# Optimization experiments

Hardware: AMD Instinct MI355X
Metric: run time of the kernel (lower is better)

Reference implementation:

```python
import jax, jax.numpy as jnp
import numpy as np


def _nn_idx(query, ref):
    """Index of nearest ref point for each query point.
    query: [B,N,3], ref: [B,M,3] -> idx [B,N] (int32).
    Squared distance via ||q||^2 - 2 q.r + ||r||^2 (matches cdist+top1).
    """
    d2 = (jnp.sum(query * query, axis=-1, keepdims=True)
          - 2.0 * jnp.einsum('bnd,bmd->bnm', query, ref)
          + jnp.sum(ref * ref, axis=-1)[:, None, :])
    return jnp.argmin(d2, axis=-1)


def setup_inputs() -> dict:
    key = jax.random.key(0)
    k1, k2, k3 = jax.random.split(key, 3)
    B, N, M = 1, 16384, 16384  # batch hard-coded to 1 in original loops
    pred = jax.random.normal(k1, (B, N, 3), dtype=jnp.float32)
    gt = jax.random.normal(k2, (B, M, 3), dtype=jnp.float32)
    weight = jax.random.uniform(k3, (1,), dtype=jnp.float32)
    return {"pred": pred, "gt": gt, "weight": weight}


def reference(pred, gt, weight):
    # get_mse_loss2: weighted bidirectional nearest-neighbor MSE.
    w = weight[0]
    # B2A: align each pred point to its nearest gt point
    idx = _nn_idx(pred, gt)                                   # [B,N]
    align_gt = jnp.take_along_axis(gt, idx[..., None], axis=1)  # [B,N,3]
    B2A = jnp.mean((pred - align_gt) ** 2)
    # A2B: align each gt point to its nearest pred point
    idx2 = _nn_idx(gt, pred)                                  # [B,M]
    align_out = jnp.take_along_axis(pred, idx2[..., None], axis=1)  # [B,M,3]
    A2B = jnp.mean((align_out - gt) ** 2)
    return B2A * w + A2B * (1.0 - w)
```

## Files before the change

### kernel.cpp

```cpp
#include <hip/hip_runtime.h>


#define NPTS   16384
#define QBLK   256
#define QCH    (NPTS / QBLK)
#define SSPLIT 8
#define RBLK   (NPTS / SSPLIT)
#define NB1    (2 * QCH * SSPLIT)

typedef __attribute__((ext_vector_type(8)))  __bf16 bf16x8;
typedef __attribute__((ext_vector_type(16))) float  floatx16;

union frag16 { __bf16 v[16]; uint4 q[2]; };

__global__ __launch_bounds__(256) void prep_kernel(
    const float* __restrict__ pred, const float* __restrict__ gt,
    uint4* __restrict__ aform, uint4* __restrict__ bform,
    float* __restrict__ out)
{
    const int i = blockIdx.x * 256 + threadIdx.x;
    if (i == 0) out[0] = 0.0f;
    const int role = (i < NPTS) ? 0 : 1;
    const int p = i - role * NPTS;
    const float* __restrict__ src = role ? gt : pred;

    const float x = src[p * 3 + 0], y = src[p * 3 + 1], z = src[p * 3 + 2];
    const float nn = x * x + y * y + z * z;
    const __bf16 xh = (__bf16)x, yh = (__bf16)y, zh = (__bf16)z;
    const __bf16 xl = (__bf16)(x - (float)xh);
    const __bf16 yl = (__bf16)(y - (float)yh);
    const __bf16 zl = (__bf16)(z - (float)zh);
    const __bf16 nh = (__bf16)nn;
    const __bf16 nl = (__bf16)(nn - (float)nh);
    const __bf16 one = (__bf16)1.0f;

    frag16 A;
    A.v[0]  = (__bf16)(-2.0f * (float)xh); A.v[1]  = A.v[0];
    A.v[2]  = (__bf16)(-2.0f * (float)xl); A.v[3]  = A.v[2];
    A.v[4]  = (__bf16)(-2.0f * (float)yh); A.v[5]  = A.v[4];
    A.v[6]  = (__bf16)(-2.0f * (float)yl); A.v[7]  = A.v[6];
    A.v[8]  = (__bf16)(-2.0f * (float)zh); A.v[9]  = A.v[8];
    A.v[10] = (__bf16)(-2.0f * (float)zl); A.v[11] = A.v[10];
    A.v[12] = nh;  A.v[13] = nl;  A.v[14] = one;  A.v[15] = one;

    frag16 B;
    B.v[0] = xh;  B.v[1]  = xl;  B.v[2]  = xh;  B.v[3]  = xl;
    B.v[4] = yh;  B.v[5]  = yl;  B.v[6]  = yh;  B.v[7]  = yl;
    B.v[8] = zh;  B.v[9]  = zl;  B.v[10] = zh;  B.v[11] = zl;
    B.v[12] = one; B.v[13] = one; B.v[14] = nh;  B.v[15] = nl;

    uint4* da = aform + (size_t)role * (NPTS * 2)
              + ((p >> 5) * 64 + (p & 31));
    da[0]  = A.q[0];
    da[32] = A.q[1];
    uint4* db = bform + (size_t)role * (NPTS * 2) + p * 2;
    db[0] = B.q[0];
    db[1] = B.q[1];
}

#define MMB(A0S, A1S, BQ, M)                                                \
    asm volatile(                                                           \
        "v_mfma_f32_32x32x16_bf16 v[32:47], " A0S ", %[B], %[Z]\n\t"        \
        "v_mfma_f32_32x32x16_bf16 v[48:63], " A1S ", %[B], %[Z]\n\t"        \
        "s_nop 7\n\ts_nop 7\n\ts_nop 7\n\ts_nop 7\n\t"                      \
        "v_min3_f32 %[M0],  %[M0],  v32, v48\n\t"                           \
        "v_min3_f32 %[M1],  %[M1],  v33, v49\n\t"                           \
        "v_min3_f32 %[M2],  %[M2],  v34, v50\n\t"                           \
        "v_min3_f32 %[M3],  %[M3],  v35, v51\n\t"                           \
        "v_min3_f32 %[M4],  %[M4],  v36, v52\n\t"                           \
        "v_min3_f32 %[M5],  %[M5],  v37, v53\n\t"                           \
        "v_min3_f32 %[M6],  %[M6],  v38, v54\n\t"                           \
        "v_min3_f32 %[M7],  %[M7],  v39, v55\n\t"                           \
        "v_min3_f32 %[M8],  %[M8],  v40, v56\n\t"                           \
        "v_min3_f32 %[M9],  %[M9],  v41, v57\n\t"                           \
        "v_min3_f32 %[M10], %[M10], v42, v58\n\t"                           \
        "v_min3_f32 %[M11], %[M11], v43, v59\n\t"                           \
        "v_min3_f32 %[M12], %[M12], v44, v60\n\t"                           \
        "v_min3_f32 %[M13], %[M13], v45, v61\n\t"                           \
        "v_min3_f32 %[M14], %[M14], v46, v62\n\t"                           \
        "v_min3_f32 %[M15], %[M15], v47, v63"                               \
        : [M0] "+v"(M[0]),  [M1] "+v"(M[1]),  [M2] "+v"(M[2]),              \
          [M3] "+v"(M[3]),  [M4] "+v"(M[4]),  [M5] "+v"(M[5]),              \
          [M6] "+v"(M[6]),  [M7] "+v"(M[7]),  [M8] "+v"(M[8]),              \
          [M9] "+v"(M[9]),  [M10] "+v"(M[10]), [M11] "+v"(M[11]),           \
          [M12] "+v"(M[12]), [M13] "+v"(M[13]), [M14] "+v"(M[14]),          \
          [M15] "+v"(M[15])                                                 \
        : [B] "v"(BQ), [Z] "v"(zero)                                        \
        : "v32", "v33", "v34", "v35", "v36", "v37", "v38", "v39",           \
          "v40", "v41", "v42", "v43", "v44", "v45", "v46", "v47",           \
          "v48", "v49", "v50", "v51", "v52", "v53", "v54", "v55",           \
          "v56", "v57", "v58", "v59", "v60", "v61", "v62", "v63")

#define ISSUE(D0S, D1S, C0, C1, C2, C3, C4, C5, C6, C7)                     \
    asm volatile(                                                           \
        "global_load_dwordx4 " D0S ", %[off], %[base]\n\t"                  \
        "global_load_dwordx4 " D1S ", %[off], %[base] offset:1024\n\t"      \
        "v_add_u32 %[off], 0x800, %[off]"                                   \
        : [off] "+v"(voff)                                                  \
        : [base] "s"(abase)                                                 \
        : C0, C1, C2, C3, C4, C5, C6, C7, "memory")

#define ISSUE0 ISSUE("v[64:67]", "v[68:71]", "v64","v65","v66","v67","v68","v69","v70","v71")
#define ISSUE1 ISSUE("v[72:75]", "v[76:79]", "v72","v73","v74","v75","v76","v77","v78","v79")
#define ISSUE2 ISSUE("v[80:83]", "v[84:87]", "v80","v81","v82","v83","v84","v85","v86","v87")
#define ISSUE3 ISSUE("v[88:91]", "v[92:95]", "v88","v89","v90","v91","v92","v93","v94","v95")

#define WAIT6 asm volatile("s_waitcnt vmcnt(6)" ::: "memory")

__global__ __launch_bounds__(256) void nn_part_kernel(
    const uint4* __restrict__ aform, const uint4* __restrict__ bform,
    float* __restrict__ partial)
{
    const int bx   = blockIdx.x;
    const int dir  = bx >> 9;
    const int qc   = (bx & 511) >> 3;
    const int s    = bx & 7;
    const int tid  = threadIdx.x;
    const int lane = tid & 63;
    const int wave = tid >> 6;
    const int lid  = lane & 31;
    const int half = lane >> 5;

    const uint4* __restrict__ Aref = aform + (size_t)(dir ? 0 : 1) * (NPTS * 2);
    const uint4* __restrict__ Bqry = bform + (size_t)(dir ? 1 : 0) * (NPTS * 2);

    const int qbase = qc * QBLK + wave * 64;
    const bf16x8 bq0 = __builtin_bit_cast(bf16x8, Bqry[(qbase + lid) * 2 + half]);
    const bf16x8 bq1 = __builtin_bit_cast(bf16x8, Bqry[(qbase + 32 + lid) * 2 + half]);

    floatx16 zero;
#pragma unroll
    for (int k = 0; k < 16; ++k) zero[k] = 0.0f;

    float ma[16], mb[16];
#pragma unroll
    for (int k = 0; k < 16; ++k) { ma[k] = 3.4e38f; mb[k] = 3.4e38f; }

    asm volatile("s_waitcnt vmcnt(0)" ::: "memory");

    const uint4* abase = Aref + (size_t)s * (RBLK * 2);
    unsigned voff = (unsigned)((half * 32 + lid) * 16);
    ISSUE0; ISSUE1; ISSUE2; ISSUE3;

    for (int j = 0; j < 8; ++j) {
        WAIT6; MMB("v[64:67]", "v[68:71]", bq0, ma);
               MMB("v[64:67]", "v[68:71]", bq1, mb); ISSUE0;
        WAIT6; MMB("v[72:75]", "v[76:79]", bq0, ma);
               MMB("v[72:75]", "v[76:79]", bq1, mb); ISSUE1;
        WAIT6; MMB("v[80:83]", "v[84:87]", bq0, ma);
               MMB("v[80:83]", "v[84:87]", bq1, mb); ISSUE2;
        WAIT6; MMB("v[88:91]", "v[92:95]", bq0, ma);
               MMB("v[88:91]", "v[92:95]", bq1, mb); ISSUE3;
    }
    asm volatile("s_waitcnt vmcnt(0)" ::: "memory");

    float* pout = partial + ((size_t)((dir * QCH + qc) * SSPLIT + s)) * QBLK
                + wave * 64;
    {
        float a = fminf(fminf(ma[0], ma[1]), fminf(ma[2], ma[3]));
        float b = fminf(fminf(ma[4], ma[5]), fminf(ma[6], ma[7]));
        float c = fminf(fminf(ma[8], ma[9]), fminf(ma[10], ma[11]));
        float d = fminf(fminf(ma[12], ma[13]), fminf(ma[14], ma[15]));
        float v = fminf(fminf(a, b), fminf(c, d));
        v = fminf(v, __shfl_xor(v, 32));
        if (half == 0) pout[lid] = v;
    }
    {
        float a = fminf(fminf(mb[0], mb[1]), fminf(mb[2], mb[3]));
        float b = fminf(fminf(mb[4], mb[5]), fminf(mb[6], mb[7]));
        float c = fminf(fminf(mb[8], mb[9]), fminf(mb[10], mb[11]));
        float d = fminf(fminf(mb[12], mb[13]), fminf(mb[14], mb[15]));
        float v = fminf(fminf(a, b), fminf(c, d));
        v = fminf(v, __shfl_xor(v, 32));
        if (half == 0) pout[32 + lid] = v;
    }
}

__global__ __launch_bounds__(256) void nn_combine_kernel(
    const float* __restrict__ partial, const float* __restrict__ weight,
    float* __restrict__ out)
{
    const int b   = blockIdx.x;
    const int dir = b >> 6;
    const int qc  = b & 63;
    const int t   = threadIdx.x;

    const float* p = partial + ((size_t)((dir * QCH + qc) * SSPLIT)) * QBLK;
    float v = p[t];
#pragma unroll
    for (int s = 1; s < SSPLIT; ++s)
        v = fminf(v, p[s * QBLK + t]);

    for (int off = 32; off; off >>= 1) v += __shfl_down(v, off);
    __shared__ float ws[4];
    if ((t & 63) == 0) ws[t >> 6] = v;
    __syncthreads();
    if (t == 0) {
        const float sum = ws[0] + ws[1] + ws[2] + ws[3];
        const float wgt = weight[0];
        const float scale = (dir ? (1.0f - wgt) : wgt) / (3.0f * (float)NPTS);
        atomicAdd(out, sum * scale);
    }
}

extern "C" void kernel_launch(void* const* d_in, const int* in_sizes, int n_in,
                              void* d_out, int out_size, void* d_ws, size_t ws_size,
                              hipStream_t stream) {
    const float* pred   = (const float*)d_in[0];
    const float* gt     = (const float*)d_in[1];
    const float* weight = (const float*)d_in[2];

    float* partial = (float*)d_ws;
    uint4* aform = (uint4*)((char*)d_ws + (size_t)2 * QCH * SSPLIT * QBLK * 4);
    uint4* bform = aform + (size_t)2 * NPTS * 2;

    prep_kernel<<<2 * NPTS / 256, 256, 0, stream>>>(pred, gt, aform, bform,
                                                    (float*)d_out);
    nn_part_kernel<<<NB1, 256, 0, stream>>>(aform, bform, partial);
    nn_combine_kernel<<<2 * QCH, 256, 0, stream>>>(partial, weight, (float*)d_out);
}
```

Baseline: 82.22 us.

## Double split count, shrink load pipeline to two stages, use inline-zero MFMA accumulator

Raises the reference-split factor from 8 to 16, which doubles the number of blocks and halves the reference points each block scans. The global-load pipeline drops from four buffers to two, with a matching vmcnt wait. The MFMA zero-accumulator registers are replaced by an inline constant 0. Together these cut VGPR use and are meant to raise occupancy and parallelism, at the cost of shallower latency hiding and more partial results for the combine kernel to merge.

```diff
diff --git a/kernel.cpp b/kernel.cpp
--- a/kernel.cpp
+++ b/kernel.cpp
@@ -4,12 +4,11 @@
 #define NPTS   16384
 #define QBLK   256
 #define QCH    (NPTS / QBLK)
-#define SSPLIT 8
+#define SSPLIT 16
 #define RBLK   (NPTS / SSPLIT)
 #define NB1    (2 * QCH * SSPLIT)
 
 typedef __attribute__((ext_vector_type(8)))  __bf16 bf16x8;
-typedef __attribute__((ext_vector_type(16))) float  floatx16;
 
 union frag16 { __bf16 v[16]; uint4 q[2]; };
 
@@ -60,8 +59,8 @@
 
 #define MMB(A0S, A1S, BQ, M)                                                \
     asm volatile(                                                           \
-        "v_mfma_f32_32x32x16_bf16 v[32:47], " A0S ", %[B], %[Z]\n\t"        \
-        "v_mfma_f32_32x32x16_bf16 v[48:63], " A1S ", %[B], %[Z]\n\t"        \
+        "v_mfma_f32_32x32x16_bf16 v[32:47], " A0S ", %[B], 0\n\t"           \
+        "v_mfma_f32_32x32x16_bf16 v[48:63], " A1S ", %[B], 0\n\t"           \
         "s_nop 7\n\ts_nop 7\n\ts_nop 7\n\ts_nop 7\n\t"                      \
         "v_min3_f32 %[M0],  %[M0],  v32, v48\n\t"                           \
         "v_min3_f32 %[M1],  %[M1],  v33, v49\n\t"                           \
@@ -85,7 +84,7 @@
           [M9] "+v"(M[9]),  [M10] "+v"(M[10]), [M11] "+v"(M[11]),           \
           [M12] "+v"(M[12]), [M13] "+v"(M[13]), [M14] "+v"(M[14]),          \
           [M15] "+v"(M[15])                                                 \
-        : [B] "v"(BQ), [Z] "v"(zero)                                        \
+        : [B] "v"(BQ)                                                       \
         : "v32", "v33", "v34", "v35", "v36", "v37", "v38", "v39",           \
           "v40", "v41", "v42", "v43", "v44", "v45", "v46", "v47",           \
           "v48", "v49", "v50", "v51", "v52", "v53", "v54", "v55",           \
@@ -100,21 +99,19 @@
         : [base] "s"(abase)                                                 \
         : C0, C1, C2, C3, C4, C5, C6, C7, "memory")
 
-#define ISSUE0 ISSUE("v[64:67]", "v[68:71]", "v64","v65","v66","v67","v68","v69","v70","v71")
-#define ISSUE1 ISSUE("v[72:75]", "v[76:79]", "v72","v73","v74","v75","v76","v77","v78","v79")
-#define ISSUE2 ISSUE("v[80:83]", "v[84:87]", "v80","v81","v82","v83","v84","v85","v86","v87")
-#define ISSUE3 ISSUE("v[88:91]", "v[92:95]", "v88","v89","v90","v91","v92","v93","v94","v95")
-
-#define WAIT6 asm volatile("s_waitcnt vmcnt(6)" ::: "memory")
+#define ISSUE_A ISSUE("v[64:67]", "v[68:71]", "v64","v65","v66","v67","v68","v69","v70","v71")
+#define ISSUE_B ISSUE("v[72:75]", "v[76:79]", "v72","v73","v74","v75","v76","v77","v78","v79")
+
+#define WAIT2 asm volatile("s_waitcnt vmcnt(2)" ::: "memory")
 
 __global__ __launch_bounds__(256) void nn_part_kernel(
     const uint4* __restrict__ aform, const uint4* __restrict__ bform,
     float* __restrict__ partial)
 {
     const int bx   = blockIdx.x;
-    const int dir  = bx >> 9;
-    const int qc   = (bx & 511) >> 3;
-    const int s    = bx & 7;
+    const int dir  = bx >> 10;
+    const int qc   = (bx >> 4) & 63;
+    const int s    = bx & 15;
     const int tid  = threadIdx.x;
     const int lane = tid & 63;
     const int wave = tid >> 6;
@@ -128,10 +125,6 @@
     const bf16x8 bq0 = __builtin_bit_cast(bf16x8, Bqry[(qbase + lid) * 2 + half]);
     const bf16x8 bq1 = __builtin_bit_cast(bf16x8, Bqry[(qbase + 32 + lid) * 2 + half]);
 
-    floatx16 zero;
-#pragma unroll
-    for (int k = 0; k < 16; ++k) zero[k] = 0.0f;
-
     float ma[16], mb[16];
 #pragma unroll
     for (int k = 0; k < 16; ++k) { ma[k] = 3.4e38f; mb[k] = 3.4e38f; }
@@ -140,17 +133,13 @@
 
     const uint4* abase = Aref + (size_t)s * (RBLK * 2);
     unsigned voff = (unsigned)((half * 32 + lid) * 16);
-    ISSUE0; ISSUE1; ISSUE2; ISSUE3;
+    ISSUE_A; ISSUE_B;
 
     for (int j = 0; j < 8; ++j) {
-        WAIT6; MMB("v[64:67]", "v[68:71]", bq0, ma);
-               MMB("v[64:67]", "v[68:71]", bq1, mb); ISSUE0;
-        WAIT6; MMB("v[72:75]", "v[76:79]", bq0, ma);
-               MMB("v[72:75]", "v[76:79]", bq1, mb); ISSUE1;
-        WAIT6; MMB("v[80:83]", "v[84:87]", bq0, ma);
-               MMB("v[80:83]", "v[84:87]", bq1, mb); ISSUE2;
-        WAIT6; MMB("v[88:91]", "v[92:95]", bq0, ma);
-               MMB("v[88:91]", "v[92:95]", bq1, mb); ISSUE3;
+        WAIT2; MMB("v[64:67]", "v[68:71]", bq0, ma);
+               MMB("v[64:67]", "v[68:71]", bq1, mb); ISSUE_A;
+        WAIT2; MMB("v[72:75]", "v[76:79]", bq0, ma);
+               MMB("v[72:75]", "v[76:79]", bq1, mb); ISSUE_B;
     }
     asm volatile("s_waitcnt vmcnt(0)" ::: "memory");
 
@@ -189,7 +178,7 @@
     float v = p[t];
 #pragma unroll
     for (int s = 1; s < SSPLIT; ++s)
-        v = fminf(v, p[s * QBLK + t]);
+        v = fminf(v, p[(size_t)s * QBLK + t]);
 
     for (int off = 32; off; off >>= 1) v += __shfl_down(v, off);
     __shared__ float ws[4];
```

After: 80.78 us. Within noise of the previous version (-1.8%).
